# Optimization experiments

Hardware: AMD Instinct MI355X
Metric: run time of the kernel (lower is better)

## Reference

```python
import jax, jax.numpy as jnp
import numpy as np

B, C, H, W = 2, 256, 96, 192
GROUPS = 4
K = 9  # search_window_1d = (1, 9) -> 9 candidates, x-offsets -4..4, y-offset 0


def bilinear_sample(img, coords):
    """F.grid_sample(mode='bilinear', padding_mode='zeros', align_corners=True)
    with absolute pixel coordinates (torchvision optical-flow grid_sample wrapper:
    normalize by 2*x/(W-1)-1 then grid_sample align_corners=True == identity mapping).
    img: [B, C, H, W]; coords: [B, Hg, Wg, 2] as (x, y). Returns [B, C, Hg, Wg]."""
    Bi, Ci, Hi, Wi = img.shape
    x = coords[..., 0]
    y = coords[..., 1]
    x0 = jnp.floor(x)
    y0 = jnp.floor(y)
    wx1 = x - x0
    wy1 = y - y0
    wx0 = 1.0 - wx1
    wy0 = 1.0 - wy1
    flat = img.reshape(Bi, Ci, Hi * Wi)

    def gather(ix, iy):
        valid = (ix >= 0) & (ix <= Wi - 1) & (iy >= 0) & (iy <= Hi - 1)
        ixc = jnp.clip(ix, 0, Wi - 1).astype(jnp.int32)
        iyc = jnp.clip(iy, 0, Hi - 1).astype(jnp.int32)
        idx = (iyc * Wi + ixc).reshape(Bi, 1, -1)  # [B,1,Hg*Wg]
        g = jnp.take_along_axis(flat, idx, axis=2)  # [B,C,Hg*Wg]
        g = g.reshape(Bi, Ci, *ix.shape[1:])
        return g * valid[:, None].astype(img.dtype)

    out = (gather(x0, y0) * (wx0 * wy0)[:, None]
           + gather(x0 + 1, y0) * (wx1 * wy0)[:, None]
           + gather(x0, y0 + 1) * (wx0 * wy1)[:, None]
           + gather(x0 + 1, y0 + 1) * (wx1 * wy1)[:, None])
    return out


def setup_inputs() -> dict:
    key = jax.random.key(0)
    k1, k2, k3, k4 = jax.random.split(key, 4)
    return {
        "left_feature": jax.random.normal(k1, (B, C, H, W), dtype=jnp.float32),
        "right_feature": jax.random.normal(k2, (B, C, H, W), dtype=jnp.float32),
        "flow": jax.random.normal(k3, (B, 2, H, W), dtype=jnp.float32),
        "extra_offset": jax.random.normal(k4, (B, 2 * K, H, W), dtype=jnp.float32),
    }


def reference(left_feature, right_feature, flow, extra_offset):
    Bf, Cf, Hf, Wf = left_feature.shape
    gc = Cf // GROUPS
    dt = left_feature.dtype
    # 1d window offsets: meshgrid(arange(-4,5), arange(0,1), 'xy') -> (x, 0) pairs
    xs = jnp.arange(-4, 5, dtype=dt)
    win_offs = jnp.stack([xs, jnp.zeros_like(xs)], axis=-1)  # [K,2] (x,y)
    # extra_offset: [B, K, 2, H, W] -> [B, K, H, W, 2]
    extra = extra_offset.reshape(Bf, K, 2, Hf, Wf).transpose(0, 1, 3, 4, 2)
    offsets = win_offs[None, :, None, None, :] + extra  # [B,K,H,W,2]
    # base coords grid (x, y) + flow
    yy, xx = jnp.meshgrid(jnp.arange(Hf), jnp.arange(Wf), indexing="ij")
    base = jnp.stack([xx, yy], axis=-1).astype(dt)  # [H,W,2]
    coords = base[None] + flow.transpose(0, 2, 3, 1)  # [B,H,W,2]
    coords = coords[:, None] + offsets  # [B,K,H,W,2]
    coords = coords.reshape(Bf, K * Hf, Wf, 2)
    # All groups share identical window/dilation -> sample full right feature once.
    sampled = bilinear_sample(right_feature, coords)  # [B,C,K*H,W]
    sampled = sampled.reshape(Bf, GROUPS, gc, K, Hf, Wf)
    left = left_feature.reshape(Bf, GROUPS, gc, 1, Hf, Wf)
    corr = jnp.mean(left * sampled, axis=2)  # [B,G,K,H,W]
    return corr.reshape(Bf, GROUPS * K, Hf, Wf)
```

## Files before the change

kernel.cpp:

```cpp
#include <hip/hip_runtime.h>


namespace {
constexpr int kB = 2;
constexpr int kC = 256;
constexpr int kH = 96;
constexpr int kW = 192;
constexpr int kG = 4;
constexpr int kGC = kC / kG;
constexpr int kK = 9;
constexpr int kHW = kH * kW;
constexpr size_t kPlane = (size_t)kC * kHW;
}

typedef _Float16 half8_t __attribute__((ext_vector_type(8)));
typedef _Float16 half4_t __attribute__((ext_vector_type(4)));
typedef _Float16 half2_t __attribute__((ext_vector_type(2)));

struct TapMeta {
  int4   off;
  float4 wgt;
};

__device__ __forceinline__ float dot8(half8_t a, half8_t b, float acc) {
#if __has_builtin(__builtin_amdgcn_fdot2)
  #pragma unroll
  for (int i = 0; i < 4; ++i) {
    half2_t a2 = {a[2 * i], a[2 * i + 1]};
    half2_t b2 = {b[2 * i], b[2 * i + 1]};
    acc = __builtin_amdgcn_fdot2(a2, b2, acc, false);
  }
#else
  #pragma unroll
  for (int i = 0; i < 8; ++i) acc += (float)a[i] * (float)b[i];
#endif
  return acc;
}

__global__ __launch_bounds__(256) void transpose_fp16(
    const float* __restrict__ left, const float* __restrict__ right,
    _Float16* __restrict__ left_t, _Float16* __restrict__ right_t)
{
  __shared__ float tile[64][65];
  int pt = blockIdx.x;
  int ct = blockIdx.y;
  int z  = blockIdx.z;
  int b  = z >> 1;
  const float* in = (z & 1) ? right : left;
  _Float16*   dst = (z & 1) ? right_t : left_t;
  int p0 = pt * 64, c0 = ct * 64;
  const float* inb = in + (size_t)b * kPlane;
  _Float16*   outb = dst + (size_t)b * kPlane;
  int t = threadIdx.x;
  int cl = t >> 2;
  int q  = t & 3;
  #pragma unroll
  for (int i = 0; i < 4; ++i) {
    int j = q + 4 * i;
    float4 v = *(const float4*)(inb + (size_t)(c0 + cl) * kHW + p0 + 4 * j);
    tile[cl][4 * j + 0] = v.x;
    tile[cl][4 * j + 1] = v.y;
    tile[cl][4 * j + 2] = v.z;
    tile[cl][4 * j + 3] = v.w;
  }
  __syncthreads();
  int pl = t >> 2;
  #pragma unroll
  for (int i = 0; i < 4; ++i) {
    int c4 = (t & 3) + 4 * i;
    half4_t hv;
    hv[0] = (_Float16)tile[4 * c4 + 0][pl];
    hv[1] = (_Float16)tile[4 * c4 + 1][pl];
    hv[2] = (_Float16)tile[4 * c4 + 2][pl];
    hv[3] = (_Float16)tile[4 * c4 + 3][pl];
    *(half4_t*)(outb + (size_t)(p0 + pl) * kC + c0 + 4 * c4) = hv;
  }
}

__global__ __launch_bounds__(256) void precompute_taps(
    const float* __restrict__ flow, const float* __restrict__ extra,
    TapMeta* __restrict__ meta)
{
  int t = blockIdx.x * blockDim.x + threadIdx.x;
  if (t >= kB * kHW) return;
  int b = t / kHW, pix = t % kHW;
  int w = pix % kW, h = pix / kW;

  const float* flowb = flow + (size_t)b * 2 * kHW + pix;
  float bx = (float)w + flowb[0];
  float by = (float)h + flowb[kHW];
  const float* extb = extra + (size_t)b * 2 * kK * kHW + pix;

  TapMeta* mp = meta + (size_t)t * kK;
  #pragma unroll
  for (int k = 0; k < kK; ++k) {
    float xx = bx + (float)(k - 4) + extb[(size_t)(2 * k) * kHW];
    float yy = by + extb[(size_t)(2 * k + 1) * kHW];
    float xf = floorf(xx), yf = floorf(yy);
    float fx = xx - xf, fy = yy - yf;
    int ix0 = (int)xf, iy0 = (int)yf;
    int ix1 = ix0 + 1, iy1 = iy0 + 1;
    bool vx0 = (ix0 >= 0) && (ix0 < kW);
    bool vx1 = (ix1 >= 0) && (ix1 < kW);
    bool vy0 = (iy0 >= 0) && (iy0 < kH);
    bool vy1 = (iy1 >= 0) && (iy1 < kH);
    int xc0 = min(max(ix0, 0), kW - 1);
    int xc1 = min(max(ix1, 0), kW - 1);
    int yc0 = min(max(iy0, 0), kH - 1);
    int yc1 = min(max(iy1, 0), kH - 1);
    float wx0 = 1.f - fx, wy0 = 1.f - fy;
    TapMeta m;
    m.off.x = (yc0 * kW + xc0) * kC;
    m.off.y = (yc0 * kW + xc1) * kC;
    m.off.z = (yc1 * kW + xc0) * kC;
    m.off.w = (yc1 * kW + xc1) * kC;
    m.wgt.x = wx0 * wy0 * ((vx0 && vy0) ? 1.f : 0.f);
    m.wgt.y = fx  * wy0 * ((vx1 && vy0) ? 1.f : 0.f);
    m.wgt.z = wx0 * fy  * ((vx0 && vy1) ? 1.f : 0.f);
    m.wgt.w = fx  * fy  * ((vx1 && vy1) ? 1.f : 0.f);
    mp[k] = m;
  }
}

__global__ __launch_bounds__(256) void corr_fp16_kernel(
    const _Float16* __restrict__ left_t, const _Float16* __restrict__ right_t,
    const TapMeta* __restrict__ meta, float* __restrict__ out)
{
  int gw   = blockIdx.x * 4 + (threadIdx.x >> 6);
  int lane = threadIdx.x & 63;
  int base = gw * 2;
  int b    = base / kHW;
  int pl0  = base % kHW;
  int p    = lane >> 5;
  int cl   = lane & 31;
  int pix  = pl0 + p;

  half8_t l8 = *(const half8_t*)(left_t + ((size_t)b * kHW + pix) * kC + cl * 8);

  const _Float16* Rb = right_t + (size_t)b * kPlane + cl * 8;
  const TapMeta* mp = meta + (size_t)(base + p) * kK;

  int g = cl >> 3;
  float* outp = out + (size_t)b * kG * kK * kHW + pix;

  #pragma unroll
  for (int k = 0; k < kK; ++k) {
    int4   off = mp[k].off;
    float4 wv  = mp[k].wgt;

    half8_t t00 = *(const half8_t*)(Rb + off.x);
    half8_t t01 = *(const half8_t*)(Rb + off.y);
    half8_t t10 = *(const half8_t*)(Rb + off.z);
    half8_t t11 = *(const half8_t*)(Rb + off.w);

    float d00 = dot8(t00, l8, 0.f);
    float d01 = dot8(t01, l8, 0.f);
    float d10 = dot8(t10, l8, 0.f);
    float d11 = dot8(t11, l8, 0.f);
    float r = wv.x * d00 + wv.y * d01 + wv.z * d10 + wv.w * d11;

    r += __shfl_xor(r, 1);
    r += __shfl_xor(r, 2);
    r += __shfl_xor(r, 4);
    if ((cl & 7) == 0)
      outp[((size_t)g * kK + k) * kHW] = r * (1.f / kGC);
  }
}

__global__ __launch_bounds__(256) void crestereo_corr_fallback(
    const float* __restrict__ left, const float* __restrict__ right,
    const float* __restrict__ flow, const float* __restrict__ extra,
    float* __restrict__ out)
{
  int t = blockIdx.x * blockDim.x + threadIdx.x;
  int w = t % kW;
  int h = (t / kW) % kH;
  int k = (t / kHW) % kK;
  int g = (t / (kHW * kK)) % kG;
  int b = t / (kHW * kK * kG);

  int pix = h * kW + w;
  const float* flowb = flow + b * 2 * kHW + pix;
  float x = (float)(w + (k - 4)) + flowb[0];
  float y = (float)h + flowb[kHW];
  const float* extb = extra + (size_t)(b * 2 * kK + 2 * k) * kHW + pix;
  x += extb[0];
  y += extb[kHW];

  float xf = floorf(x), yf = floorf(y);
  float fx = x - xf, fy = y - yf;
  int ix0 = (int)xf, iy0 = (int)yf;
  int ix1 = ix0 + 1, iy1 = iy0 + 1;
  bool vx0 = (ix0 >= 0) && (ix0 < kW);
  bool vx1 = (ix1 >= 0) && (ix1 < kW);
  bool vy0 = (iy0 >= 0) && (iy0 < kH);
  bool vy1 = (iy1 >= 0) && (iy1 < kH);
  int xc0 = min(max(ix0, 0), kW - 1);
  int xc1 = min(max(ix1, 0), kW - 1);
  int yc0 = min(max(iy0, 0), kH - 1);
  int yc1 = min(max(iy1, 0), kH - 1);
  float wx0 = 1.f - fx, wy0 = 1.f - fy;
  float w00 = wx0 * wy0 * ((vx0 && vy0) ? 1.f : 0.f);
  float w01 = fx  * wy0 * ((vx1 && vy0) ? 1.f : 0.f);
  float w10 = wx0 * fy  * ((vx0 && vy1) ? 1.f : 0.f);
  float w11 = fx  * fy  * ((vx1 && vy1) ? 1.f : 0.f);
  int idx = yc0 * kW + xc0;
  int dx  = xc1 - xc0;
  int dyw = (yc1 - yc0) * kW;

  const float* Rb = right + (size_t)(b * kC + g * kGC) * kHW + idx;
  const float* Lb = left  + (size_t)(b * kC + g * kGC) * kHW + pix;

  float acc = 0.f;
  #pragma unroll 4
  for (int c = 0; c < kGC; ++c) {
    const float* Rc = Rb + (size_t)c * kHW;
    float l   = Lb[(size_t)c * kHW];
    acc += l * (w00 * Rc[0] + w01 * Rc[dx] + w10 * Rc[dyw] + w11 * Rc[dx + dyw]);
  }
  out[(size_t)((b * kG + g) * kK + k) * kHW + pix] = acc * (1.f / kGC);
}

extern "C" void kernel_launch(void* const* d_in, const int* in_sizes, int n_in,
                              void* d_out, int out_size, void* d_ws, size_t ws_size,
                              hipStream_t stream) {
  const float* left  = (const float*)d_in[0];
  const float* right = (const float*)d_in[1];
  const float* flow  = (const float*)d_in[2];
  const float* extra = (const float*)d_in[3];
  float* out = (float*)d_out;

  size_t t_bytes = 2 * (size_t)kB * kPlane * sizeof(_Float16);
  size_t m_bytes = (size_t)kB * kHW * kK * sizeof(TapMeta);
  if (ws_size >= t_bytes + m_bytes) {
    _Float16* left_t  = (_Float16*)d_ws;
    _Float16* right_t = left_t + (size_t)kB * kPlane;
    TapMeta*  meta    = (TapMeta*)((char*)d_ws + t_bytes);

    dim3 tgrid(kHW / 64, kC / 64, kB * 2);
    transpose_fp16<<<tgrid, 256, 0, stream>>>(left, right, left_t, right_t);
    precompute_taps<<<(kB * kHW + 255) / 256, 256, 0, stream>>>(flow, extra, meta);
    int waves = kB * kHW / 2;
    corr_fp16_kernel<<<waves / 4, 256, 0, stream>>>(left_t, right_t, meta, out);
  } else {
    int total = kB * kG * kK * kH * kW;
    crestereo_corr_fallback<<<(total + 255) / 256, 256, 0, stream>>>(
        left, right, flow, extra, out);
  }
}
```

Measured before the change: 158.2 us.

## Merge transpose and tap precompute into one prepass; batch tap gathers in corr kernel

The fp16 transpose and the bilinear tap-metadata kernels are combined into a single launch that picks its role from the block index, removing one kernel launch and the gap between them. The correlation kernel now issues the gathers for three taps at a time before doing the dot products, to raise memory-level parallelism, and writes all nine outputs at the end from the leader lanes. This raises register pressure in the correlation kernel, and the merged prepass mixes blocks with different resource needs: every block, including the tap-compute ones, declares the shared-memory tile.

```diff
diff --git a/kernel.cpp b/kernel.cpp
--- a/kernel.cpp
+++ b/kernel.cpp
@@ -11,6 +11,8 @@
 constexpr int kK = 9;
 constexpr int kHW = kH * kW;
 constexpr size_t kPlane = (size_t)kC * kHW;
+constexpr int kTransBlocks = (kHW / 64) * (kC / 64) * kB * 2;
+constexpr int kPreBlocks   = (kB * kHW) / 256;
 }
 
 typedef _Float16 half8_t __attribute__((ext_vector_type(8)));
@@ -37,88 +39,87 @@
   return acc;
 }
 
-__global__ __launch_bounds__(256) void transpose_fp16(
+__global__ __launch_bounds__(256) void prepass_kernel(
     const float* __restrict__ left, const float* __restrict__ right,
-    _Float16* __restrict__ left_t, _Float16* __restrict__ right_t)
+    const float* __restrict__ flow, const float* __restrict__ extra,
+    _Float16* __restrict__ left_t, _Float16* __restrict__ right_t,
+    TapMeta* __restrict__ meta)
 {
   __shared__ float tile[64][65];
-  int pt = blockIdx.x;
-  int ct = blockIdx.y;
-  int z  = blockIdx.z;
-  int b  = z >> 1;
-  const float* in = (z & 1) ? right : left;
-  _Float16*   dst = (z & 1) ? right_t : left_t;
-  int p0 = pt * 64, c0 = ct * 64;
-  const float* inb = in + (size_t)b * kPlane;
-  _Float16*   outb = dst + (size_t)b * kPlane;
-  int t = threadIdx.x;
-  int cl = t >> 2;
-  int q  = t & 3;
-  #pragma unroll
-  for (int i = 0; i < 4; ++i) {
-    int j = q + 4 * i;
-    float4 v = *(const float4*)(inb + (size_t)(c0 + cl) * kHW + p0 + 4 * j);
-    tile[cl][4 * j + 0] = v.x;
-    tile[cl][4 * j + 1] = v.y;
-    tile[cl][4 * j + 2] = v.z;
-    tile[cl][4 * j + 3] = v.w;
-  }
-  __syncthreads();
-  int pl = t >> 2;
-  #pragma unroll
-  for (int i = 0; i < 4; ++i) {
-    int c4 = (t & 3) + 4 * i;
-    half4_t hv;
-    hv[0] = (_Float16)tile[4 * c4 + 0][pl];
-    hv[1] = (_Float16)tile[4 * c4 + 1][pl];
-    hv[2] = (_Float16)tile[4 * c4 + 2][pl];
-    hv[3] = (_Float16)tile[4 * c4 + 3][pl];
-    *(half4_t*)(outb + (size_t)(p0 + pl) * kC + c0 + 4 * c4) = hv;
-  }
-}
-
-__global__ __launch_bounds__(256) void precompute_taps(
-    const float* __restrict__ flow, const float* __restrict__ extra,
-    TapMeta* __restrict__ meta)
-{
-  int t = blockIdx.x * blockDim.x + threadIdx.x;
-  if (t >= kB * kHW) return;
-  int b = t / kHW, pix = t % kHW;
-  int w = pix % kW, h = pix / kW;
-
-  const float* flowb = flow + (size_t)b * 2 * kHW + pix;
-  float bx = (float)w + flowb[0];
-  float by = (float)h + flowb[kHW];
-  const float* extb = extra + (size_t)b * 2 * kK * kHW + pix;
-
-  TapMeta* mp = meta + (size_t)t * kK;
-  #pragma unroll
-  for (int k = 0; k < kK; ++k) {
-    float xx = bx + (float)(k - 4) + extb[(size_t)(2 * k) * kHW];
-    float yy = by + extb[(size_t)(2 * k + 1) * kHW];
-    float xf = floorf(xx), yf = floorf(yy);
-    float fx = xx - xf, fy = yy - yf;
-    int ix0 = (int)xf, iy0 = (int)yf;
-    int ix1 = ix0 + 1, iy1 = iy0 + 1;
-    bool vx0 = (ix0 >= 0) && (ix0 < kW);
-    bool vx1 = (ix1 >= 0) && (ix1 < kW);
-    bool vy0 = (iy0 >= 0) && (iy0 < kH);
-    bool vy1 = (iy1 >= 0) && (iy1 < kH);
-    int xc0 = min(max(ix0, 0), kW - 1);
-    int xc1 = min(max(ix1, 0), kW - 1);
-    int yc0 = min(max(iy0, 0), kH - 1);
-    int yc1 = min(max(iy1, 0), kH - 1);
-    float wx0 = 1.f - fx, wy0 = 1.f - fy;
-    TapMeta m;
-    m.off.x = (yc0 * kW + xc0) * kC;
-    m.off.y = (yc0 * kW + xc1) * kC;
-    m.off.z = (yc1 * kW + xc0) * kC;
-    m.off.w = (yc1 * kW + xc1) * kC;
-    m.wgt.x = wx0 * wy0 * ((vx0 && vy0) ? 1.f : 0.f);
-    m.wgt.y = fx  * wy0 * ((vx1 && vy0) ? 1.f : 0.f);
-    m.wgt.z = wx0 * fy  * ((vx0 && vy1) ? 1.f : 0.f);
-    m.wgt.w = fx  * fy  * ((vx1 && vy1) ? 1.f : 0.f);
-    mp[k] = m;
+  int id = blockIdx.x;
+  if (id < kTransBlocks) {
+    int pt = id % (kHW / 64);
+    int ct = (id / (kHW / 64)) % 4;
+    int z  = id / ((kHW / 64) * 4);
+    int b  = z >> 1;
+    const float* in = (z & 1) ? right : left;
+    _Float16*   dst = (z & 1) ? right_t : left_t;
+    int p0 = pt * 64, c0 = ct * 64;
+    const float* inb = in + (size_t)b * kPlane;
+    _Float16*   outb = dst + (size_t)b * kPlane;
+    int t = threadIdx.x;
+    int cl = t >> 2;
+    int q  = t & 3;
+    #pragma unroll
+    for (int i = 0; i < 4; ++i) {
+      int j = q + 4 * i;
+      float4 v = *(const float4*)(inb + (size_t)(c0 + cl) * kHW + p0 + 4 * j);
+      tile[cl][4 * j + 0] = v.x;
+      tile[cl][4 * j + 1] = v.y;
+      tile[cl][4 * j + 2] = v.z;
+      tile[cl][4 * j + 3] = v.w;
+    }
+    __syncthreads();
+    int pl = t >> 2;
+    #pragma unroll
+    for (int i = 0; i < 4; ++i) {
+      int c4 = (t & 3) + 4 * i;
+      half4_t hv;
+      hv[0] = (_Float16)tile[4 * c4 + 0][pl];
+      hv[1] = (_Float16)tile[4 * c4 + 1][pl];
+      hv[2] = (_Float16)tile[4 * c4 + 2][pl];
+      hv[3] = (_Float16)tile[4 * c4 + 3][pl];
+      *(half4_t*)(outb + (size_t)(p0 + pl) * kC + c0 + 4 * c4) = hv;
+    }
+  } else {
+    int t = (id - kTransBlocks) * 256 + threadIdx.x;
+    int b = t / kHW, pix = t % kHW;
+    int w = pix % kW, h = pix / kW;
+
+    const float* flowb = flow + (size_t)b * 2 * kHW + pix;
+    float bx = (float)w + flowb[0];
+    float by = (float)h + flowb[kHW];
+    const float* extb = extra + (size_t)b * 2 * kK * kHW + pix;
+
+    TapMeta* mp = meta + (size_t)t * kK;
+    #pragma unroll
+    for (int k = 0; k < kK; ++k) {
+      float xx = bx + (float)(k - 4) + extb[(size_t)(2 * k) * kHW];
+      float yy = by + extb[(size_t)(2 * k + 1) * kHW];
+      float xf = floorf(xx), yf = floorf(yy);
+      float fx = xx - xf, fy = yy - yf;
+      int ix0 = (int)xf, iy0 = (int)yf;
+      int ix1 = ix0 + 1, iy1 = iy0 + 1;
+      bool vx0 = (ix0 >= 0) && (ix0 < kW);
+      bool vx1 = (ix1 >= 0) && (ix1 < kW);
+      bool vy0 = (iy0 >= 0) && (iy0 < kH);
+      bool vy1 = (iy1 >= 0) && (iy1 < kH);
+      int xc0 = min(max(ix0, 0), kW - 1);
+      int xc1 = min(max(ix1, 0), kW - 1);
+      int yc0 = min(max(iy0, 0), kH - 1);
+      int yc1 = min(max(iy1, 0), kH - 1);
+      float wx0 = 1.f - fx, wy0 = 1.f - fy;
+      TapMeta m;
+      m.off.x = (yc0 * kW + xc0) * kC;
+      m.off.y = (yc0 * kW + xc1) * kC;
+      m.off.z = (yc1 * kW + xc0) * kC;
+      m.off.w = (yc1 * kW + xc1) * kC;
+      m.wgt.x = wx0 * wy0 * ((vx0 && vy0) ? 1.f : 0.f);
+      m.wgt.y = fx  * wy0 * ((vx1 && vy0) ? 1.f : 0.f);
+      m.wgt.z = wx0 * fy  * ((vx0 && vy1) ? 1.f : 0.f);
+      m.wgt.w = fx  * fy  * ((vx1 && vy1) ? 1.f : 0.f);
+      mp[k] = m;
+    }
   }
 }
 
@@ -140,30 +141,45 @@
   const _Float16* Rb = right_t + (size_t)b * kPlane + cl * 8;
   const TapMeta* mp = meta + (size_t)(base + p) * kK;
 
+  float rr[kK];
+
+  #pragma unroll
+  for (int kb = 0; kb < kK; kb += 3) {
+    int4   off[3];
+    float4 wv[3];
+    #pragma unroll
+    for (int j = 0; j < 3; ++j) {
+      off[j] = mp[kb + j].off;
+      wv[j]  = mp[kb + j].wgt;
+    }
+    half8_t t[3][4];
+    #pragma unroll
+    for (int j = 0; j < 3; ++j) {
+      t[j][0] = *(const half8_t*)(Rb + off[j].x);
+      t[j][1] = *(const half8_t*)(Rb + off[j].y);
+      t[j][2] = *(const half8_t*)(Rb + off[j].z);
+      t[j][3] = *(const half8_t*)(Rb + off[j].w);
+    }
+    #pragma unroll
+    for (int j = 0; j < 3; ++j) {
+      float d00 = dot8(t[j][0], l8, 0.f);
+      float d01 = dot8(t[j][1], l8, 0.f);
+      float d10 = dot8(t[j][2], l8, 0.f);
+      float d11 = dot8(t[j][3], l8, 0.f);
+      float r = wv[j].x * d00 + wv[j].y * d01 + wv[j].z * d10 + wv[j].w * d11;
+      r += __shfl_xor(r, 1);
+      r += __shfl_xor(r, 2);
+      r += __shfl_xor(r, 4);
+      rr[kb + j] = r;
+    }
+  }
+
   int g = cl >> 3;
-  float* outp = out + (size_t)b * kG * kK * kHW + pix;
-
-  #pragma unroll
-  for (int k = 0; k < kK; ++k) {
-    int4   off = mp[k].off;
-    float4 wv  = mp[k].wgt;
-
-    half8_t t00 = *(const half8_t*)(Rb + off.x);
-    half8_t t01 = *(const half8_t*)(Rb + off.y);
-    half8_t t10 = *(const half8_t*)(Rb + off.z);
-    half8_t t11 = *(const half8_t*)(Rb + off.w);
-
-    float d00 = dot8(t00, l8, 0.f);
-    float d01 = dot8(t01, l8, 0.f);
-    float d10 = dot8(t10, l8, 0.f);
-    float d11 = dot8(t11, l8, 0.f);
-    float r = wv.x * d00 + wv.y * d01 + wv.z * d10 + wv.w * d11;
-
-    r += __shfl_xor(r, 1);
-    r += __shfl_xor(r, 2);
-    r += __shfl_xor(r, 4);
-    if ((cl & 7) == 0)
-      outp[((size_t)g * kK + k) * kHW] = r * (1.f / kGC);
+  if ((cl & 7) == 0) {
+    float* outp = out + ((size_t)b * kG + g) * kK * kHW + pix;
+    #pragma unroll
+    for (int k = 0; k < kK; ++k)
+      outp[(size_t)k * kHW] = rr[k] * (1.f / kGC);
   }
 }
 
@@ -237,9 +253,8 @@
     _Float16* right_t = left_t + (size_t)kB * kPlane;
     TapMeta*  meta    = (TapMeta*)((char*)d_ws + t_bytes);
 
-    dim3 tgrid(kHW / 64, kC / 64, kB * 2);
-    transpose_fp16<<<tgrid, 256, 0, stream>>>(left, right, left_t, right_t);
-    precompute_taps<<<(kB * kHW + 255) / 256, 256, 0, stream>>>(flow, extra, meta);
+    prepass_kernel<<<kTransBlocks + kPreBlocks, 256, 0, stream>>>(
+        left, right, flow, extra, left_t, right_t, meta);
     int waves = kB * kHW / 2;
     corr_fp16_kernel<<<waves / 4, 256, 0, stream>>>(left_t, right_t, meta, out);
   } else {
```

Measured after the change: 159.8 us. No clear change (+1.0%).
